# Performance work log

Hardware: AMD Instinct MI355X
Metric: run time of the kernel (lower is better)

The kernel has to match this reference:

```python
import jax, jax.numpy as jnp
import numpy as np
from jax import lax

_A = -0.75  # PyTorch bicubic coefficient


def _cubic_kernel(x):
    x = np.abs(x)
    return np.where(x <= 1.0, (_A + 2) * x**3 - (_A + 3) * x**2 + 1,
                    np.where(x < 2.0, _A * x**3 - 5 * _A * x**2 + 8 * _A * x - 4 * _A, 0.0))


def _cubic_mat(out_s, in_s):
    # align_corners=True bicubic interpolation matrix [out_s, in_s]
    i = np.arange(out_s)
    s = i * (in_s - 1) / (out_s - 1) if out_s > 1 else np.zeros(out_s)
    f = np.floor(s).astype(np.int64)
    t = s - f
    M = np.zeros((out_s, in_s), dtype=np.float32)
    for off in range(-1, 3):
        idx = np.clip(f + off, 0, in_s - 1)
        np.add.at(M, (i, idx), _cubic_kernel(t - off).astype(np.float32))
    return jnp.asarray(M)


def _bicubic_up(x, out_hw):
    Mh = _cubic_mat(out_hw[0], x.shape[-2])
    Mw = _cubic_mat(out_hw[1], x.shape[-1])
    y = jnp.einsum('Hh,bchw->bcHw', Mh, x)
    return jnp.einsum('Ww,bcHw->bcHW', Mw, y)


def _conv(x, w, b, pad=1):
    y = lax.conv_general_dilated(x, w, (1, 1), [(pad, pad), (pad, pad)],
                                 dimension_numbers=('NCHW', 'OIHW', 'NCHW'))
    return y + b[None, :, None, None]


def _pool(x):
    return lax.reduce_window(x, -jnp.inf, lax.max, (1, 1, 2, 2), (1, 1, 2, 2), 'VALID')


def _features(x, ws):
    # VGG19 feat1 = conv0+relu (64ch, full res); feat2 = conv2..conv14 (256ch, 1/4 res)
    x1 = jax.nn.relu(_conv(x, *ws[0]))
    h = jax.nn.relu(_conv(x1, *ws[1]))
    h = _pool(h)
    h = jax.nn.relu(_conv(h, *ws[2]))
    h = jax.nn.relu(_conv(h, *ws[3]))
    h = _pool(h)
    h = jax.nn.relu(_conv(h, *ws[4]))
    h = jax.nn.relu(_conv(h, *ws[5]))
    h = jax.nn.relu(_conv(h, *ws[6]))
    h = _bicubic_up(h, x1.shape[-2:])  # bicubic, align_corners=True
    return jnp.concatenate([x1, h], axis=1)  # 64 + 256 = 320 channels


def _forward(x_ref, x_template, w0, b0, w2, b2, w5, b5, w7, b7, w10, b10, w12, b12,
             w14, b14, coef_ref, coef_temp, fw1, fb1, fw2, fb2, fw3, fb3):
    ws = [(w0, b0), (w2, b2), (w5, b5), (w7, b7), (w10, b10), (w12, b12), (w14, b14)]
    fref = _features(x_ref, ws)
    ftem = _features(x_template, ws)
    # L2-normalize over channel dim
    fref = fref / (1e-8 + jnp.linalg.norm(fref, axis=1, keepdims=True))
    ftem = ftem / (1e-8 + jnp.linalg.norm(ftem, axis=1, keepdims=True))
    b, c, H, W = fref.shape
    fref = fref.reshape(b, c, H // 2, 2, W // 2, 2).mean(axis=(3, 5))
    # dense correlation volume
    dist = jnp.einsum('bcmn,bcpq->bmnpq', fref, ftem) / 320.0
    m, n, p, q = dist.shape[1:]
    dist = dist.reshape(b, m * n, p * q)
    # dual-axis softmax + sqrt combination (LoFTR-style)
    conf_ref = jax.nn.softmax(coef_ref * dist, axis=-2)
    conf_tmp = jax.nn.softmax(coef_temp * dist, axis=-1)
    confidence = jnp.sqrt(conf_ref * conf_tmp)
    conf_values, _ = lax.top_k(confidence, 5)  # [b, m*n, 5]
    conf = conf_values.reshape(b, m, n, 5).transpose(0, 3, 1, 2)
    # final head (dropout = identity in eval)
    h = jax.nn.relu(_conv(conf, fw1, fb1))
    h = jax.nn.relu(_conv(h, fw2, fb2))
    out = _conv(h, fw3, fb3, pad=0)
    out = _bicubic_up(out, x_ref.shape[-2:])
    return out


def setup_inputs() -> dict:
    key = jax.random.key(0)
    ks = jax.random.split(key, 16)
    B, H, W = 1, 128, 128

    def cw(k, o, i, s):
        return jax.random.normal(k, (o, i, s, s), jnp.float32) * (1.0 / np.sqrt(i * s * s))

    d = {
        'x_ref': jax.random.normal(ks[0], (B, 3, H, W), jnp.float32),
        'x_template': jax.random.normal(ks[1], (B, 3, H, W), jnp.float32),
        'w0': cw(ks[2], 64, 3, 3), 'b0': jnp.zeros((64,), jnp.float32),
        'w2': cw(ks[3], 64, 64, 3), 'b2': jnp.zeros((64,), jnp.float32),
        'w5': cw(ks[4], 128, 64, 3), 'b5': jnp.zeros((128,), jnp.float32),
        'w7': cw(ks[5], 128, 128, 3), 'b7': jnp.zeros((128,), jnp.float32),
        'w10': cw(ks[6], 256, 128, 3), 'b10': jnp.zeros((256,), jnp.float32),
        'w12': cw(ks[7], 256, 256, 3), 'b12': jnp.zeros((256,), jnp.float32),
        'w14': cw(ks[8], 256, 256, 3), 'b14': jnp.zeros((256,), jnp.float32),
        'coef_ref': jnp.float32(1.0), 'coef_temp': jnp.float32(1.0),
        # final head: weights_init_normal -> N(1/3, 0.02)
        'fw1': 1.0 / 3 + 0.02 * jax.random.normal(ks[9], (8, 5, 3, 3), jnp.float32),
        'fb1': 0.02 * jax.random.normal(ks[10], (8,), jnp.float32),
        'fw2': 1.0 / 3 + 0.02 * jax.random.normal(ks[11], (8, 8, 3, 3), jnp.float32),
        'fb2': 0.02 * jax.random.normal(ks[12], (8,), jnp.float32),
        'fw3': 1.0 / 3 + 0.02 * jax.random.normal(ks[13], (1, 8, 1, 1), jnp.float32),
        'fb3': 0.02 * jax.random.normal(ks[14], (1,), jnp.float32),
    }
    return d


def reference(x_ref, x_template, w0, b0, w2, b2, w5, b5, w7, b7, w10, b10, w12, b12,
              w14, b14, coef_ref, coef_temp, fw1, fb1, fw2, fb2, fw3, fb3):
    return _forward(x_ref, x_template, w0, b0, w2, b2, w5, b5, w7, b7, w10, b10,
                    w12, b12, w14, b14, coef_ref, coef_temp, fw1, fb1, fw2, fb2, fw3, fb3)
```

## Files before the change

### kernel.cpp

```cpp
#include <hip/hip_runtime.h>
#include <math.h>

typedef unsigned short ushort_t;
typedef unsigned int uint_t;
typedef __attribute__((ext_vector_type(8))) short bf16x8;
typedef __attribute__((ext_vector_type(4))) float f32x4;

#define FSTRIDE ((size_t)16384 * 320)
#define TSTRIDE ((size_t)16384 * 64)

__device__ inline ushort_t f2bf(float f) {
    union { float f; uint_t u; } x; x.f = f;
    uint_t r = x.u + 0x7fffu + ((x.u >> 16) & 1u);
    return (ushort_t)(r >> 16);
}
__device__ inline float bf2f(ushort_t h) {
    union { uint_t u; float f; } x; x.u = ((uint_t)h) << 16;
    return x.f;
}
__device__ inline float bflo(uint_t u) {
    union { uint_t u; float f; } x; x.u = u << 16; return x.f;
}
__device__ inline float bfhi(uint_t u) {
    union { uint_t u; float f; } x; x.u = u & 0xffff0000u; return x.f;
}

struct WT6 {
    const float* src[6];
    ushort_t* dst[6];
    int co[6], ci[6];
    int off[6];
};
__global__ void wtrans6_k(WT6 a)
{
    int b = blockIdx.x, seg = 0;
#pragma unroll
    for (int s = 1; s < 6; ++s) if (b >= a.off[s]) seg = s;
    int idx = (b - a.off[seg]) * 256 + threadIdx.x;
    int CO = a.co[seg], CI = a.ci[seg];
    if (idx >= CO * CI * 9) return;
    int tap = idx % 9;
    int rem = idx / 9;
    int ci = rem % CI;
    int co = rem / CI;
    a.dst[seg][((size_t)tap * CO + co) * CI + ci] = f2bf(a.src[seg][idx]);
}

__global__ __launch_bounds__(256) void conv0_k(const float* __restrict__ x0, const float* __restrict__ x1,
                                               const float* __restrict__ w,
                                               const float* __restrict__ b, ushort_t* __restrict__ F,
                                               ushort_t* __restrict__ t0)
{
    const float* x = blockIdx.y ? x1 : x0;
    F += (size_t)blockIdx.y * FSTRIDE;
    t0 += (size_t)blockIdx.y * TSTRIDE;
    int co = threadIdx.x & 63;
    int p = blockIdx.x * 4 + (threadIdx.x >> 6);
    int y = p >> 7, xx = p & 127;
    float acc = b[co];
#pragma unroll
    for (int ci = 0; ci < 3; ++ci) {
#pragma unroll
        for (int t = 0; t < 9; ++t) {
            int dy = t / 3 - 1, dx = t % 3 - 1;
            int yy = y + dy, xc = xx + dx;
            if ((unsigned)yy < 128u && (unsigned)xc < 128u) {
                acc += x[ci * 16384 + yy * 128 + xc] * w[co * 27 + ci * 9 + t];
            }
        }
    }
    ushort_t r = f2bf(fmaxf(acc, 0.f));
    F[(size_t)p * 320 + co] = r;
    t0[(size_t)p * 64 + co] = r;
}

template<int CI>
__global__ __launch_bounds__(256) void conv_mfma_k(
    const ushort_t* __restrict__ in, int ldin, int inoff, size_t inImgStride,
    const ushort_t* __restrict__ wT, const float* __restrict__ bias,
    ushort_t* __restrict__ out, int ldout, int outoff, size_t outImgStride,
    int H, int W, int CO)
{
    in += (size_t)blockIdx.z * inImgStride;
    out += (size_t)blockIdx.z * outImgStride;
    const int tid = threadIdx.x;
    const int lane = tid & 63, wid = tid >> 6;
    const int wr = wid >> 1, wc = wid & 1;
    const int m0 = blockIdx.x * 64;
    const int n0 = blockIdx.y * 64;
    const int fr = lane & 15;
    const int fo = (lane >> 4) << 3;

    size_t abase[2];
    unsigned vmask[2];
#pragma unroll
    for (int mi = 0; mi < 2; ++mi) {
        int p = m0 + wr * 32 + mi * 16 + fr;
        int y = p / W, x = p % W;
        abase[mi] = (size_t)p * ldin + inoff + fo;
        unsigned vm = 0;
#pragma unroll
        for (int t = 0; t < 9; ++t) {
            int dy = t / 3 - 1, dx = t % 3 - 1;
            if ((unsigned)(y + dy) < (unsigned)H && (unsigned)(x + dx) < (unsigned)W) vm |= 1u << t;
        }
        vmask[mi] = vm;
    }

    f32x4 zero = {0.f, 0.f, 0.f, 0.f};
    f32x4 acc[2][2] = {{zero, zero}, {zero, zero}};
    const bf16x8 zz = {0, 0, 0, 0, 0, 0, 0, 0};

    for (int t = 0; t < 9; ++t) {
        int toff = ((t / 3 - 1) * W + (t % 3 - 1)) * ldin;
        bool v0 = (vmask[0] >> t) & 1u;
        bool v1 = (vmask[1] >> t) & 1u;
        const ushort_t* wp0 = wT + ((size_t)(t * CO + n0 + wc * 32 + fr)) * CI + fo;
        const ushort_t* wp1 = wp0 + (size_t)16 * CI;
#pragma unroll
        for (int kc = 0; kc < CI / 32; ++kc) {
            int k0 = kc * 32;
            bf16x8 a0 = v0 ? *(const bf16x8*)(in + abase[0] + toff + k0) : zz;
            bf16x8 a1 = v1 ? *(const bf16x8*)(in + abase[1] + toff + k0) : zz;
            bf16x8 b0 = *(const bf16x8*)(wp0 + k0);
            bf16x8 b1 = *(const bf16x8*)(wp1 + k0);
            acc[0][0] = __builtin_amdgcn_mfma_f32_16x16x32_bf16(b0, a0, acc[0][0], 0, 0, 0);
            acc[0][1] = __builtin_amdgcn_mfma_f32_16x16x32_bf16(b1, a0, acc[0][1], 0, 0, 0);
            acc[1][0] = __builtin_amdgcn_mfma_f32_16x16x32_bf16(b0, a1, acc[1][0], 0, 0, 0);
            acc[1][1] = __builtin_amdgcn_mfma_f32_16x16x32_bf16(b1, a1, acc[1][1], 0, 0, 0);
        }
    }

#pragma unroll
    for (int mi = 0; mi < 2; ++mi) {
#pragma unroll
        for (int ni = 0; ni < 2; ++ni) {
            int pix = m0 + wr * 32 + mi * 16 + (lane & 15);
            int ch = n0 + wc * 32 + ni * 16 + ((lane >> 4) << 2);
            float4 bv = *(const float4*)(bias + ch);
            float r0 = fmaxf(acc[mi][ni][0] + bv.x, 0.f);
            float r1 = fmaxf(acc[mi][ni][1] + bv.y, 0.f);
            float r2 = fmaxf(acc[mi][ni][2] + bv.z, 0.f);
            float r3 = fmaxf(acc[mi][ni][3] + bv.w, 0.f);
            uint2 pk;
            pk.x = (uint_t)f2bf(r0) | ((uint_t)f2bf(r1) << 16);
            pk.y = (uint_t)f2bf(r2) | ((uint_t)f2bf(r3) << 16);
            *(uint2*)(out + (size_t)pix * ldout + outoff + ch) = pk;
        }
    }
}

template<int CI>
__global__ __launch_bounds__(128) void conv_mfma2w_k(
    const ushort_t* __restrict__ in, int ldin, size_t inImgStride,
    const ushort_t* __restrict__ wT, const float* __restrict__ bias,
    ushort_t* __restrict__ out, int ldout, size_t outImgStride,
    int H, int W, int CO)
{
    __shared__ float red[64][17];
    in += (size_t)blockIdx.z * inImgStride;
    out += (size_t)blockIdx.z * outImgStride;
    const int lane = threadIdx.x & 63;
    const int wv = threadIdx.x >> 6;
    const int m0 = blockIdx.x * 32;
    const int n0 = blockIdx.y * 32;
    const int fr = lane & 15;
    const int fo = (lane >> 4) << 3;

    size_t abase[2];
    unsigned vmask[2];
#pragma unroll
    for (int mi = 0; mi < 2; ++mi) {
        int p = m0 + mi * 16 + fr;
        int y = p / W, x = p % W;
        abase[mi] = (size_t)p * ldin + fo;
        unsigned vm = 0;
#pragma unroll
        for (int t = 0; t < 9; ++t) {
            int dy = t / 3 - 1, dx = t % 3 - 1;
            if ((unsigned)(y + dy) < (unsigned)H && (unsigned)(x + dx) < (unsigned)W) vm |= 1u << t;
        }
        vmask[mi] = vm;
    }

    f32x4 zero = {0.f, 0.f, 0.f, 0.f};
    f32x4 acc[2][2] = {{zero, zero}, {zero, zero}};
    const bf16x8 zz = {0, 0, 0, 0, 0, 0, 0, 0};

    const int tb = wv ? 5 : 0;
    const int te = wv ? 9 : 5;
    for (int t = tb; t < te; ++t) {
        int toff = ((t / 3 - 1) * W + (t % 3 - 1)) * ldin;
        bool v0 = (vmask[0] >> t) & 1u;
        bool v1 = (vmask[1] >> t) & 1u;
        const ushort_t* wp0 = wT + ((size_t)(t * CO + n0 + fr)) * CI + fo;
        const ushort_t* wp1 = wp0 + (size_t)16 * CI;
#pragma unroll
        for (int kc = 0; kc < CI / 32; ++kc) {
            int k0 = kc * 32;
            bf16x8 a0 = v0 ? *(const bf16x8*)(in + abase[0] + toff + k0) : zz;
            bf16x8 a1 = v1 ? *(const bf16x8*)(in + abase[1] + toff + k0) : zz;
            bf16x8 b0 = *(const bf16x8*)(wp0 + k0);
            bf16x8 b1 = *(const bf16x8*)(wp1 + k0);
            acc[0][0] = __builtin_amdgcn_mfma_f32_16x16x32_bf16(b0, a0, acc[0][0], 0, 0, 0);
            acc[0][1] = __builtin_amdgcn_mfma_f32_16x16x32_bf16(b1, a0, acc[0][1], 0, 0, 0);
            acc[1][0] = __builtin_amdgcn_mfma_f32_16x16x32_bf16(b0, a1, acc[1][0], 0, 0, 0);
            acc[1][1] = __builtin_amdgcn_mfma_f32_16x16x32_bf16(b1, a1, acc[1][1], 0, 0, 0);
        }
    }

    if (wv == 1) {
#pragma unroll
        for (int mi = 0; mi < 2; ++mi)
#pragma unroll
            for (int ni = 0; ni < 2; ++ni)
#pragma unroll
                for (int r = 0; r < 4; ++r)
                    red[lane][mi * 8 + ni * 4 + r] = acc[mi][ni][r];
    }
    __syncthreads();
    if (wv == 0) {
#pragma unroll
        for (int mi = 0; mi < 2; ++mi) {
#pragma unroll
            for (int ni = 0; ni < 2; ++ni) {
                int pix = m0 + mi * 16 + (lane & 15);
                int ch = n0 + ni * 16 + ((lane >> 4) << 2);
                float4 bv = *(const float4*)(bias + ch);
                float r0 = fmaxf(acc[mi][ni][0] + red[lane][mi * 8 + ni * 4 + 0] + bv.x, 0.f);
                float r1 = fmaxf(acc[mi][ni][1] + red[lane][mi * 8 + ni * 4 + 1] + bv.y, 0.f);
                float r2 = fmaxf(acc[mi][ni][2] + red[lane][mi * 8 + ni * 4 + 2] + bv.z, 0.f);
                float r3 = fmaxf(acc[mi][ni][3] + red[lane][mi * 8 + ni * 4 + 3] + bv.w, 0.f);
                uint2 pk;
                pk.x = (uint_t)f2bf(r0) | ((uint_t)f2bf(r1) << 16);
                pk.y = (uint_t)f2bf(r2) | ((uint_t)f2bf(r3) << 16);
                *(uint2*)(out + (size_t)pix * ldout + ch) = pk;
            }
        }
    }
}

__global__ void maxpool_nhwc_k(const ushort_t* __restrict__ in, ushort_t* __restrict__ out,
                               int C, int Hi, int Wi)
{
    in += (size_t)blockIdx.y * TSTRIDE;
    out += (size_t)blockIdx.y * TSTRIDE;
    int idx = blockIdx.x * 256 + threadIdx.x;
    int CG = C >> 3;
    int Wo = Wi >> 1, Ho = Hi >> 1;
    if (idx >= Ho * Wo * CG) return;
    int cg = idx % CG;
    int p = idx / CG;
    int y = p / Wo, x = p % Wo;
    const ushort_t* ip = in + ((size_t)(2 * y) * Wi + 2 * x) * C + cg * 8;
    bf16x8 v0 = *(const bf16x8*)(ip);
    bf16x8 v1 = *(const bf16x8*)(ip + C);
    bf16x8 v2 = *(const bf16x8*)(ip + (size_t)Wi * C);
    bf16x8 v3 = *(const bf16x8*)(ip + (size_t)Wi * C + C);
    bf16x8 r;
#pragma unroll
    for (int j = 0; j < 8; ++j) {
        float m = fmaxf(fmaxf(bf2f((ushort_t)v0[j]), bf2f((ushort_t)v1[j])),
                        fmaxf(bf2f((ushort_t)v2[j]), bf2f((ushort_t)v3[j])));
        r[j] = (short)f2bf(m);
    }
    *(bf16x8*)(out + (size_t)p * C + cg * 8) = r;
}

__device__ inline void cubw(float t, float* w) {
    float x0 = 1.f + t, x2 = 1.f - t, x3 = 2.f - t;
    w[0] = ((-0.75f*x0 + 3.75f)*x0 - 6.f)*x0 + 3.f;
    w[1] = (1.25f*t - 2.25f)*t*t + 1.f;
    w[2] = (1.25f*x2 - 2.25f)*x2*x2 + 1.f;
    w[3] = ((-0.75f*x3 + 3.75f)*x3 - 6.f)*x3 + 3.f;
}

__global__ __launch_bounds__(256) void upnorm_k(const ushort_t* __restrict__ in, ushort_t* __restrict__ F,
                                                ushort_t* __restrict__ Abuf)
{
    __shared__ float sm[4][320];
    in += (size_t)blockIdx.y * TSTRIDE;
    F += (size_t)blockIdx.y * FSTRIDE;
    int wid = threadIdx.x >> 6, lane = threadIdx.x & 63;
    int pb = blockIdx.x;
    int py = pb >> 6, px = pb & 63;
    int p = (2 * py + (wid >> 1)) * 128 + 2 * px + (wid & 1);
    int Y = p >> 7, X = p & 127;
    float sy = (float)Y * (31.f / 127.f);
    float sx = (float)X * (31.f / 127.f);
    int fy = (int)floorf(sy), fx = (int)floorf(sx);
    float ty = sy - (float)fy, tx = sx - (float)fx;
    float wy[4], wx[4];
    cubw(ty, wy); cubw(tx, wx);
    float a0 = 0.f, a1 = 0.f, a2 = 0.f, a3 = 0.f;
#pragma unroll
    for (int i = 0; i < 4; ++i) {
        int yy = min(max(fy - 1 + i, 0), 31);
#pragma unroll
        for (int j = 0; j < 4; ++j) {
            int xx = min(max(fx - 1 + j, 0), 31);
            float w = wy[i] * wx[j];
            uint2 v = *(const uint2*)(in + ((size_t)yy * 32 + xx) * 256 + lane * 4);
            a0 += w * bflo(v.x); a1 += w * bfhi(v.x);
            a2 += w * bflo(v.y); a3 += w * bfhi(v.y);
        }
    }
    float v0 = bf2f(f2bf(a0)), v1 = bf2f(f2bf(a1)), v2 = bf2f(f2bf(a2)), v3 = bf2f(f2bf(a3));
    float c0 = bf2f(F[(size_t)p * 320 + lane]);
    float ss = c0 * c0 + v0 * v0 + v1 * v1 + v2 * v2 + v3 * v3;
#pragma unroll
    for (int off = 32; off > 0; off >>= 1) ss += __shfl_xor(ss, off);
    float inv = 1.f / (1e-8f + sqrtf(ss));
    if (blockIdx.y == 1) {
        F[(size_t)p * 320 + lane] = f2bf(c0 * inv);
        uint2 pk;
        pk.x = (uint_t)f2bf(v0 * inv) | ((uint_t)f2bf(v1 * inv) << 16);
        pk.y = (uint_t)f2bf(v2 * inv) | ((uint_t)f2bf(v3 * inv) << 16);
        *(uint2*)(F + (size_t)p * 320 + 64 + lane * 4) = pk;
    } else {
        sm[wid][lane] = bf2f(f2bf(c0 * inv));
        sm[wid][64 + lane * 4 + 0] = bf2f(f2bf(v0 * inv));
        sm[wid][64 + lane * 4 + 1] = bf2f(f2bf(v1 * inv));
        sm[wid][64 + lane * 4 + 2] = bf2f(f2bf(v2 * inv));
        sm[wid][64 + lane * 4 + 3] = bf2f(f2bf(v3 * inv));
        __syncthreads();
        for (int ch = threadIdx.x; ch < 320; ch += 256) {
            float a = 0.25f * (sm[0][ch] + sm[1][ch] + sm[2][ch] + sm[3][ch]);
            Abuf[(size_t)pb * 320 + ch] = f2bf(a);
        }
    }
}

__global__ __launch_bounds__(256) void gemm_corr_k(
    const ushort_t* __restrict__ A, const ushort_t* __restrict__ B, char* __restrict__ D8,
    const float* __restrict__ coefr, const float* __restrict__ coeft,
    float* __restrict__ rpsum, float* __restrict__ cpsum)
{
    __shared__ ushort_t lA0[128 * 32];
    __shared__ ushort_t lB0[128 * 32];
    __shared__ ushort_t lA1[128 * 32];
    __shared__ ushort_t lB1[128 * 32];
    __shared__ float cl[2][128];
    __shared__ float rl[2][128];
    const int tid = threadIdx.x;
    const int lane = tid & 63;
    const int wid = tid >> 6;
    const int wr = wid >> 1, wc = wid & 1;
    const int m0 = blockIdx.y * 128, n0 = blockIdx.x * 128;
    const int fr = lane & 15;
    const int fo = (lane >> 4) << 3;
    const int srow = tid >> 2;
    const int scol = (tid & 3) << 3;

    const ushort_t* Ag0 = A + (size_t)(m0 + srow) * 320 + scol;
    const ushort_t* Ag1 = Ag0 + (size_t)64 * 320;
    const ushort_t* Bg0 = B + (size_t)(n0 + srow) * 320 + scol;
    const ushort_t* Bg1 = Bg0 + (size_t)64 * 320;

    f32x4 zero = {0.f, 0.f, 0.f, 0.f};
    f32x4 acc[4][4];
#pragma unroll
    for (int i = 0; i < 4; ++i)
#pragma unroll
        for (int j = 0; j < 4; ++j) acc[i][j] = zero;

    uint4 pA0, pA1, pB0, pB1;
    uint4 qA0, qA1, qB0, qB1;

#define GLOAD(rA0, rA1, rB0, rB1, kk) { \
        rA0 = *(const uint4*)(Ag0 + (kk)); \
        rA1 = *(const uint4*)(Ag1 + (kk)); \
        rB0 = *(const uint4*)(Bg0 + (kk)); \
        rB1 = *(const uint4*)(Bg1 + (kk)); }

#define DSW(LA, LB, rA0, rA1, rB0, rB1) { \
        *(uint4*)&LA[srow * 32 + scol] = rA0; \
        *(uint4*)&LA[(64 + srow) * 32 + scol] = rA1; \
        *(uint4*)&LB[srow * 32 + scol] = rB0; \
        *(uint4*)&LB[(64 + srow) * 32 + scol] = rB1; }

#define CMP(LA, LB) { \
        bf16x8 af[4], bfr[4]; \
        _Pragma("unroll") \
        for (int mi = 0; mi < 4; ++mi) \
            af[mi] = *(const bf16x8*)&LA[(wr * 64 + mi * 16 + fr) * 32 + fo]; \
        _Pragma("unroll") \
        for (int ni = 0; ni < 4; ++ni) \
            bfr[ni] = *(const bf16x8*)&LB[(wc * 64 + ni * 16 + fr) * 32 + fo]; \
        _Pragma("unroll") \
        for (int mi = 0; mi < 4; ++mi) \
            _Pragma("unroll") \
            for (int ni = 0; ni < 4; ++ni) \
                acc[mi][ni] = __builtin_amdgcn_mfma_f32_16x16x32_bf16(bfr[ni], af[mi], acc[mi][ni], 0, 0, 0); }

    GLOAD(pA0, pA1, pB0, pB1, 0)
    DSW(lA0, lB0, pA0, pA1, pB0, pB1)
    __syncthreads();

#pragma unroll
    for (int tt = 0; tt < 5; ++tt) {
        GLOAD(qA0, qA1, qB0, qB1, 32 * (2 * tt + 1))
        CMP(lA0, lB0)
        DSW(lA1, lB1, qA0, qA1, qB0, qB1)
        __syncthreads();
        if (tt < 4) {
            GLOAD(pA0, pA1, pB0, pB1, 32 * (2 * tt + 2))
            CMP(lA1, lB1)
            DSW(lA0, lB0, pA0, pA1, pB0, pB1)
            __syncthreads();
        } else {
            CMP(lA1, lB1)
        }
    }
#undef GLOAD
#undef DSW
#undef CMP

    const float s = 1.0f / 320.0f;
    const float cr = coefr[0], ct = coeft[0];
    const bool sameCoef = (cr == ct);
    float rpx[4] = {0.f, 0.f, 0.f, 0.f};
    float cpx[4][4];
#pragma unroll
    for (int ni = 0; ni < 4; ++ni)
#pragma unroll
        for (int r = 0; r < 4; ++r) cpx[ni][r] = 0.f;

    const int mrow = lane & 15;
    const int ng = (lane >> 4) << 2;
#pragma unroll
    for (int mi = 0; mi < 4; ++mi) {
        int m = m0 + wr * 64 + mi * 16 + mrow;
        char* drow = D8 + (size_t)m * 16384;
#pragma unroll
        for (int ni = 0; ni < 4; ++ni) {
            int n = n0 + wc * 64 + ni * 16 + ng;
            float d0 = acc[mi][ni][0] * s;
            float d1 = acc[mi][ni][1] * s;
            float d2 = acc[mi][ni][2] * s;
            float d3 = acc[mi][ni][3] * s;
            int q0 = __float2int_rn(fminf(fmaxf(d0 * 40640.f, -127.f), 127.f));
            int q1 = __float2int_rn(fminf(fmaxf(d1 * 40640.f, -127.f), 127.f));
            int q2 = __float2int_rn(fminf(fmaxf(d2 * 40640.f, -127.f), 127.f));
            int q3 = __float2int_rn(fminf(fmaxf(d3 * 40640.f, -127.f), 127.f));
            uint_t pk8 = (uint_t)(q0 & 255) | ((uint_t)(q1 & 255) << 8)
                       | ((uint_t)(q2 & 255) << 16) | ((uint_t)(q3 & 255) << 24);
            *(uint_t*)(drow + n) = pk8;
            float e0 = __expf(cr * d0), e1 = __expf(cr * d1);
            float e2 = __expf(cr * d2), e3 = __expf(cr * d3);
            cpx[ni][0] += e0; cpx[ni][1] += e1; cpx[ni][2] += e2; cpx[ni][3] += e3;
            if (sameCoef) {
                rpx[mi] += e0 + e1 + e2 + e3;
            } else {
                rpx[mi] += __expf(ct * d0) + __expf(ct * d1) + __expf(ct * d2) + __expf(ct * d3);
            }
        }
    }
#pragma unroll
    for (int mi = 0; mi < 4; ++mi) {
        rpx[mi] += __shfl_xor(rpx[mi], 16);
        rpx[mi] += __shfl_xor(rpx[mi], 32);
    }
    if (lane < 16) {
#pragma unroll
        for (int mi = 0; mi < 4; ++mi)
            rl[wc][wr * 64 + mi * 16 + lane] = rpx[mi];
    }
#pragma unroll
    for (int ni = 0; ni < 4; ++ni)
#pragma unroll
        for (int r = 0; r < 4; ++r) {
            cpx[ni][r] += __shfl_xor(cpx[ni][r], 1);
            cpx[ni][r] += __shfl_xor(cpx[ni][r], 2);
            cpx[ni][r] += __shfl_xor(cpx[ni][r], 4);
            cpx[ni][r] += __shfl_xor(cpx[ni][r], 8);
        }
    if ((lane & 15) == 0) {
        int g = lane >> 4;
#pragma unroll
        for (int ni = 0; ni < 4; ++ni)
#pragma unroll
            for (int r = 0; r < 4; ++r)
                cl[wr][wc * 64 + ni * 16 + g * 4 + r] = cpx[ni][r];
    }
    __syncthreads();
    if (tid < 128) {
        cpsum[(size_t)blockIdx.y * 16384 + n0 + tid] = cl[0][tid] + cl[1][tid];
        rpsum[(size_t)blockIdx.x * 4096 + m0 + tid] = rl[0][tid] + rl[1][tid];
    }
}

__global__ void finboth_k(const float* __restrict__ cpsum, const float* __restrict__ rpsum,
                          float* __restrict__ lc, float* __restrict__ invr)
{
    int b = blockIdx.x;
    if (b < 64) {
        int j = b * 256 + threadIdx.x;
        float s = 0.f;
#pragma unroll
        for (int k = 0; k < 32; ++k) s += cpsum[(size_t)k * 16384 + j];
        lc[j] = -0.5f * __logf(s);
    } else {
        int m = (b - 64) * 256 + threadIdx.x;
        float s = 0.f;
#pragma unroll
        for (int k = 0; k < 128; ++k) s += rpsum[(size_t)k * 4096 + m];
        invr[m] = rsqrtf(s);
    }
}

#define INS5(w_) { float w = (w_); float mx; \
    mx = fmaxf(w, t0); w = fminf(w, t0); t0 = mx; \
    mx = fmaxf(w, t1); w = fminf(w, t1); t1 = mx; \
    mx = fmaxf(w, t2); w = fminf(w, t2); t2 = mx; \
    mx = fmaxf(w, t3); w = fminf(w, t3); t3 = mx; \
    t4 = fmaxf(w, t4); }
#define SB(w, sft) ((float)(int)(signed char)(((w) >> (sft)) & 0xffu))

__global__ __launch_bounds__(256) void row_topk_k(
    const char* __restrict__ D8, const float* __restrict__ lc,
    const float* __restrict__ invr,
    const float* __restrict__ coefr, const float* __restrict__ coeft,
    float* __restrict__ conf5)
{
    int wid = threadIdx.x >> 6, lane = threadIdx.x & 63;
    int row = blockIdx.x * 4 + wid;
    float hc = 0.5f * (coefr[0] + coeft[0]);
    float hq = hc * (1.0f / 40640.f);
    const char* rp = D8 + (size_t)row * 16384;

    float t0 = -1e30f, t1 = -1e30f, t2 = -1e30f, t3 = -1e30f, t4 = -1e30f;
    for (int i = 0; i < 16; ++i) {
        int cw = i * 64 + lane;
        uint4 u = *(const uint4*)(rp + cw * 16);
        int col = cw * 16;
        float4 l0 = *(const float4*)(lc + col);
        float4 l1 = *(const float4*)(lc + col + 4);
        float4 l2 = *(const float4*)(lc + col + 8);
        float4 l3 = *(const float4*)(lc + col + 12);
        float k0  = fmaf(hq, SB(u.x, 0),  l0.x);
        float k1  = fmaf(hq, SB(u.x, 8),  l0.y);
        float k2  = fmaf(hq, SB(u.x, 16), l0.z);
        float k3  = fmaf(hq, SB(u.x, 24), l0.w);
        float k4  = fmaf(hq, SB(u.y, 0),  l1.x);
        float k5  = fmaf(hq, SB(u.y, 8),  l1.y);
        float k6  = fmaf(hq, SB(u.y, 16), l1.z);
        float k7  = fmaf(hq, SB(u.y, 24), l1.w);
        float k8  = fmaf(hq, SB(u.z, 0),  l2.x);
        float k9  = fmaf(hq, SB(u.z, 8),  l2.y);
        float k10 = fmaf(hq, SB(u.z, 16), l2.z);
        float k11 = fmaf(hq, SB(u.z, 24), l2.w);
        float k12 = fmaf(hq, SB(u.w, 0),  l3.x);
        float k13 = fmaf(hq, SB(u.w, 8),  l3.y);
        float k14 = fmaf(hq, SB(u.w, 16), l3.z);
        float k15 = fmaf(hq, SB(u.w, 24), l3.w);
        float ma = fmaxf(fmaxf(fmaxf(k0, k1), fmaxf(k2, k3)),
                         fmaxf(fmaxf(k4, k5), fmaxf(k6, k7)));
        float mb = fmaxf(fmaxf(fmaxf(k8, k9), fmaxf(k10, k11)),
                         fmaxf(fmaxf(k12, k13), fmaxf(k14, k15)));
        if (fmaxf(ma, mb) > t4) {
            INS5(k0);  INS5(k1);  INS5(k2);  INS5(k3);
            INS5(k4);  INS5(k5);  INS5(k6);  INS5(k7);
            INS5(k8);  INS5(k9);  INS5(k10); INS5(k11);
            INS5(k12); INS5(k13); INS5(k14); INS5(k15);
        }
    }
#pragma unroll
    for (int off = 1; off < 64; off <<= 1) {
        float o0 = __shfl_xor(t0, off), o1 = __shfl_xor(t1, off), o2 = __shfl_xor(t2, off);
        float o3 = __shfl_xor(t3, off), o4 = __shfl_xor(t4, off);
        INS5(o0); INS5(o1); INS5(o2); INS5(o3); INS5(o4);
    }
    if (lane == 0) {
        float iv = invr[row];
        conf5[0 * 4096 + row] = __expf(t0) * iv;
        conf5[1 * 4096 + row] = __expf(t1) * iv;
        conf5[2 * 4096 + row] = __expf(t2) * iv;
        conf5[3 * 4096 + row] = __expf(t3) * iv;
        conf5[4 * 4096 + row] = __expf(t4) * iv;
    }
}

__global__ void conv3x3_k(const float* __restrict__ in, const float* __restrict__ wgt,
                          const float* __restrict__ bias, float* __restrict__ out,
                          int Cin, int H, int W, int relu)
{
    int p = blockIdx.x * 256 + threadIdx.x;
    int HW = H * W;
    if (p >= HW) return;
    int co0 = blockIdx.y * 8;
    int y = p / W, x = p - y * W;
    float acc0 = bias[co0+0], acc1 = bias[co0+1], acc2 = bias[co0+2], acc3 = bias[co0+3];
    float acc4 = bias[co0+4], acc5 = bias[co0+5], acc6 = bias[co0+6], acc7 = bias[co0+7];
    bool ym = y > 0, yp = y < H-1, xm = x > 0, xp = x < W-1;
    for (int ci = 0; ci < Cin; ++ci) {
        const float* ip = in + (size_t)ci * HW + p;
        float v0 = (ym && xm) ? ip[-W-1] : 0.f;
        float v1 = (ym)       ? ip[-W]   : 0.f;
        float v2 = (ym && xp) ? ip[-W+1] : 0.f;
        float v3 = (xm)       ? ip[-1]   : 0.f;
        float v4 =              ip[0];
        float v5 = (xp)       ? ip[1]    : 0.f;
        float v6 = (yp && xm) ? ip[W-1]  : 0.f;
        float v7 = (yp)       ? ip[W]    : 0.f;
        float v8 = (yp && xp) ? ip[W+1]  : 0.f;
        const float* wp = wgt + ((size_t)co0 * Cin + ci) * 9;
        size_t ws = (size_t)Cin * 9;
#define CACC(q, a) { const float* wq = wp + q * ws; \
        a += wq[0]*v0 + wq[1]*v1 + wq[2]*v2 + wq[3]*v3 + wq[4]*v4 \
           + wq[5]*v5 + wq[6]*v6 + wq[7]*v7 + wq[8]*v8; }
        CACC(0, acc0) CACC(1, acc1) CACC(2, acc2) CACC(3, acc3)
        CACC(4, acc4) CACC(5, acc5) CACC(6, acc6) CACC(7, acc7)
#undef CACC
    }
#define CW(q, a) { float r = a; if (relu) r = fmaxf(r, 0.f); out[(size_t)(co0+q)*HW + p] = r; }
    CW(0, acc0) CW(1, acc1) CW(2, acc2) CW(3, acc3)
    CW(4, acc4) CW(5, acc5) CW(6, acc6) CW(7, acc7)
#undef CW
}

__global__ void head2_k(const float* __restrict__ in, const float* __restrict__ wgt,
                        const float* __restrict__ bias, const float* __restrict__ w3,
                        const float* __restrict__ b3, float* __restrict__ out64)
{
    int p = blockIdx.x * 256 + threadIdx.x;
    int y = p >> 6, x = p & 63;
    float acc[8];
#pragma unroll
    for (int c = 0; c < 8; ++c) acc[c] = bias[c];
    bool ym = y > 0, yp = y < 63, xm = x > 0, xp = x < 63;
#pragma unroll
    for (int ci = 0; ci < 8; ++ci) {
        const float* ip = in + ci * 4096 + p;
        float v0 = (ym && xm) ? ip[-65] : 0.f;
        float v1 = (ym)       ? ip[-64] : 0.f;
        float v2 = (ym && xp) ? ip[-63] : 0.f;
        float v3 = (xm)       ? ip[-1]  : 0.f;
        float v4 =              ip[0];
        float v5 = (xp)       ? ip[1]   : 0.f;
        float v6 = (yp && xm) ? ip[63]  : 0.f;
        float v7 = (yp)       ? ip[64]  : 0.f;
        float v8 = (yp && xp) ? ip[65]  : 0.f;
#pragma unroll
        for (int co = 0; co < 8; ++co) {
            const float* wq = wgt + ((size_t)co * 8 + ci) * 9;
            acc[co] += wq[0]*v0 + wq[1]*v1 + wq[2]*v2 + wq[3]*v3 + wq[4]*v4
                     + wq[5]*v5 + wq[6]*v6 + wq[7]*v7 + wq[8]*v8;
        }
    }
    float o = b3[0];
#pragma unroll
    for (int c = 0; c < 8; ++c) o += w3[c] * fmaxf(acc[c], 0.f);
    out64[p] = o;
}

__global__ void bicubic_k(const float* __restrict__ in, float* __restrict__ out,
                          int C, int Hin, int Win, int Hout, int Wout)
{
    int idx = blockIdx.x * 256 + threadIdx.x;
    int total = C * Hout * Wout;
    if (idx >= total) return;
    int X = idx % Wout;
    int Y = (idx / Wout) % Hout;
    int c = idx / (Wout * Hout);
    float sy = (float)Y * (float)(Hin - 1) / (float)(Hout - 1);
    float sx = (float)X * (float)(Win - 1) / (float)(Wout - 1);
    int fy = (int)floorf(sy), fx = (int)floorf(sx);
    float ty = sy - (float)fy, tx = sx - (float)fx;
    float wy[4], wx[4];
    cubw(ty, wy); cubw(tx, wx);
    const float* ip = in + (size_t)c * Hin * Win;
    float acc = 0.f;
#pragma unroll
    for (int i = 0; i < 4; ++i) {
        int yy = min(max(fy - 1 + i, 0), Hin - 1);
        float ra = 0.f;
#pragma unroll
        for (int j = 0; j < 4; ++j) {
            int xx = min(max(fx - 1 + j, 0), Hin == Win ? Win - 1 : Win - 1);
            ra += wx[j] * ip[yy * Win + xx];
        }
        acc += wy[i] * ra;
    }
    out[idx] = acc;
}

extern "C" void kernel_launch(void* const* d_in, const int* in_sizes, int n_in,
                              void* d_out, int out_size, void* d_ws, size_t ws_size,
                              hipStream_t stream)
{
    const float* x_ref = (const float*)d_in[0];
    const float* x_tem = (const float*)d_in[1];
    const float* w0  = (const float*)d_in[2];   const float* b0  = (const float*)d_in[3];
    const float* w2  = (const float*)d_in[4];   const float* b2  = (const float*)d_in[5];
    const float* w5  = (const float*)d_in[6];   const float* b5  = (const float*)d_in[7];
    const float* w7  = (const float*)d_in[8];   const float* b7  = (const float*)d_in[9];
    const float* w10 = (const float*)d_in[10];  const float* b10 = (const float*)d_in[11];
    const float* w12 = (const float*)d_in[12];  const float* b12 = (const float*)d_in[13];
    const float* w14 = (const float*)d_in[14];  const float* b14 = (const float*)d_in[15];
    const float* coefr = (const float*)d_in[16];
    const float* coeft = (const float*)d_in[17];
    const float* fw1 = (const float*)d_in[18];  const float* fb1 = (const float*)d_in[19];
    const float* fw2 = (const float*)d_in[20];  const float* fb2 = (const float*)d_in[21];
    const float* fw3 = (const float*)d_in[22];  const float* fb3 = (const float*)d_in[23];
    float* out = (float*)d_out;

    char* wsp = (char*)d_ws;
    auto alloc = [&](size_t bytes) { char* p = wsp; wsp += (bytes + 255) & ~(size_t)255; return p; };
    ushort_t* F     = (ushort_t*)alloc(2 * FSTRIDE * 2);
    ushort_t* t0    = (ushort_t*)alloc(2 * TSTRIDE * 2);
    ushort_t* t1    = (ushort_t*)alloc(2 * TSTRIDE * 2);
    ushort_t* t2    = (ushort_t*)alloc(2 * TSTRIDE * 2);
    ushort_t* wT2   = (ushort_t*)alloc((size_t)64 * 64 * 9 * 2);
    ushort_t* wT5   = (ushort_t*)alloc((size_t)128 * 64 * 9 * 2);
    ushort_t* wT7   = (ushort_t*)alloc((size_t)128 * 128 * 9 * 2);
    ushort_t* wT10  = (ushort_t*)alloc((size_t)256 * 128 * 9 * 2);
    ushort_t* wT12  = (ushort_t*)alloc((size_t)256 * 256 * 9 * 2);
    ushort_t* wT14  = (ushort_t*)alloc((size_t)256 * 256 * 9 * 2);
    ushort_t* Abuf  = (ushort_t*)alloc((size_t)4096 * 320 * 2);
    char*     dist8 = (char*)alloc((size_t)4096 * 16384);
    float*    rpsum = (float*)alloc((size_t)128 * 4096 * 4);
    float*    cpsum = (float*)alloc((size_t)32 * 16384 * 4);
    float*    lc    = (float*)alloc(16384 * 4);
    float*    invr  = (float*)alloc(4096 * 4);
    float*    conf5 = (float*)alloc(5 * 4096 * 4);
    float*    h1    = (float*)alloc(8 * 4096 * 4);
    float*    out64 = (float*)alloc(4096 * 4);
    (void)ws_size; (void)n_in; (void)in_sizes; (void)out_size;

    WT6 wt;
    wt.src[0] = w2;  wt.dst[0] = wT2;  wt.co[0] = 64;  wt.ci[0] = 64;
    wt.src[1] = w5;  wt.dst[1] = wT5;  wt.co[1] = 128; wt.ci[1] = 64;
    wt.src[2] = w7;  wt.dst[2] = wT7;  wt.co[2] = 128; wt.ci[2] = 128;
    wt.src[3] = w10; wt.dst[3] = wT10; wt.co[3] = 256; wt.ci[3] = 128;
    wt.src[4] = w12; wt.dst[4] = wT12; wt.co[4] = 256; wt.ci[4] = 256;
    wt.src[5] = w14; wt.dst[5] = wT14; wt.co[5] = 256; wt.ci[5] = 256;
    int nblk = 0;
    for (int s = 0; s < 6; ++s) { wt.off[s] = nblk; nblk += (wt.co[s] * wt.ci[s] * 9 + 255) / 256; }
    wtrans6_k<<<nblk, 256, 0, stream>>>(wt);

    conv0_k<<<dim3(4096, 2), 256, 0, stream>>>(x_ref, x_tem, w0, b0, F, t0);
    conv_mfma_k<64><<<dim3(256, 1, 2), 256, 0, stream>>>(t0, 64, 0, TSTRIDE, wT2, b2, t1, 64, 0, TSTRIDE, 128, 128, 64);
    maxpool_nhwc_k<<<dim3(128, 2), 256, 0, stream>>>(t1, t2, 64, 128, 128);
    conv_mfma_k<64><<<dim3(64, 2, 2), 256, 0, stream>>>(t2, 64, 0, TSTRIDE, wT5, b5, t1, 128, 0, TSTRIDE, 64, 64, 128);
    conv_mfma_k<128><<<dim3(64, 2, 2), 256, 0, stream>>>(t1, 128, 0, TSTRIDE, wT7, b7, t2, 128, 0, TSTRIDE, 64, 64, 128);
    maxpool_nhwc_k<<<dim3(64, 2), 256, 0, stream>>>(t2, t1, 128, 64, 64);
    conv_mfma2w_k<128><<<dim3(32, 8, 2), 128, 0, stream>>>(t1, 128, TSTRIDE, wT10, b10, t2, 256, TSTRIDE, 32, 32, 256);
    conv_mfma2w_k<256><<<dim3(32, 8, 2), 128, 0, stream>>>(t2, 256, TSTRIDE, wT12, b12, t1, 256, TSTRIDE, 32, 32, 256);
    conv_mfma2w_k<256><<<dim3(32, 8, 2), 128, 0, stream>>>(t1, 256, TSTRIDE, wT14, b14, t2, 256, TSTRIDE, 32, 32, 256);
    upnorm_k<<<dim3(4096, 2), 256, 0, stream>>>(t2, F, Abuf);

    gemm_corr_k<<<dim3(128, 32), 256, 0, stream>>>(Abuf, F + FSTRIDE, dist8, coefr, coeft, rpsum, cpsum);

    finboth_k<<<80, 256, 0, stream>>>(cpsum, rpsum, lc, invr);

    row_topk_k<<<1024, 256, 0, stream>>>(dist8, lc, invr, coefr, coeft, conf5);

    conv3x3_k<<<dim3(16, 1), 256, 0, stream>>>(conf5, fw1, fb1, h1, 5, 64, 64, 1);
    head2_k<<<16, 256, 0, stream>>>(h1, fw2, fb2, fw3, fb3, out64);
    bicubic_k<<<64, 256, 0, stream>>>(out64, out, 1, 64, 64, 128, 128);
}
```

Before: 386.6 us.

## Restructure correlation GEMM to keep A panel resident in LDS and stream B

The correlation GEMM now runs 512 blocks. Each block loads a full 64x320 A panel into padded LDS once, then loops over 2048 columns of B, loading B fragments directly from global memory into registers without LDS staging or barriers. The grid is swizzled so that neighbouring blocks share B columns. Partial-sum layouts change to match: 64 column partials and 8 row partials, and the finalize kernel is updated accordingly. This removes the per-K-step LDS double buffering and syncs, but B is read from global with less reuse, and the serial 16-iteration loop per block lowers parallelism.

```diff
diff --git a/kernel.cpp b/kernel.cpp
--- a/kernel.cpp
+++ b/kernel.cpp
@@ -336,157 +336,124 @@
     const float* __restrict__ coefr, const float* __restrict__ coeft,
     float* __restrict__ rpsum, float* __restrict__ cpsum)
 {
-    __shared__ ushort_t lA0[128 * 32];
-    __shared__ ushort_t lB0[128 * 32];
-    __shared__ ushort_t lA1[128 * 32];
-    __shared__ ushort_t lB1[128 * 32];
-    __shared__ float cl[2][128];
-    __shared__ float rl[2][128];
+    __shared__ ushort_t lA[64 * 328];
+    __shared__ float rl[4][64];
     const int tid = threadIdx.x;
     const int lane = tid & 63;
-    const int wid = tid >> 6;
-    const int wr = wid >> 1, wc = wid & 1;
-    const int m0 = blockIdx.y * 128, n0 = blockIdx.x * 128;
+    const int wv = tid >> 6;
     const int fr = lane & 15;
     const int fo = (lane >> 4) << 3;
-    const int srow = tid >> 2;
-    const int scol = (tid & 3) << 3;
-
-    const ushort_t* Ag0 = A + (size_t)(m0 + srow) * 320 + scol;
-    const ushort_t* Ag1 = Ag0 + (size_t)64 * 320;
-    const ushort_t* Bg0 = B + (size_t)(n0 + srow) * 320 + scol;
-    const ushort_t* Bg1 = Bg0 + (size_t)64 * 320;
-
-    f32x4 zero = {0.f, 0.f, 0.f, 0.f};
-    f32x4 acc[4][4];
-#pragma unroll
-    for (int i = 0; i < 4; ++i)
-#pragma unroll
-        for (int j = 0; j < 4; ++j) acc[i][j] = zero;
-
-    uint4 pA0, pA1, pB0, pB1;
-    uint4 qA0, qA1, qB0, qB1;
-
-#define GLOAD(rA0, rA1, rB0, rB1, kk) { \
-        rA0 = *(const uint4*)(Ag0 + (kk)); \
-        rA1 = *(const uint4*)(Ag1 + (kk)); \
-        rB0 = *(const uint4*)(Bg0 + (kk)); \
-        rB1 = *(const uint4*)(Bg1 + (kk)); }
-
-#define DSW(LA, LB, rA0, rA1, rB0, rB1) { \
-        *(uint4*)&LA[srow * 32 + scol] = rA0; \
-        *(uint4*)&LA[(64 + srow) * 32 + scol] = rA1; \
-        *(uint4*)&LB[srow * 32 + scol] = rB0; \
-        *(uint4*)&LB[(64 + srow) * 32 + scol] = rB1; }
-
-#define CMP(LA, LB) { \
-        bf16x8 af[4], bfr[4]; \
-        _Pragma("unroll") \
-        for (int mi = 0; mi < 4; ++mi) \
-            af[mi] = *(const bf16x8*)&LA[(wr * 64 + mi * 16 + fr) * 32 + fo]; \
-        _Pragma("unroll") \
-        for (int ni = 0; ni < 4; ++ni) \
-            bfr[ni] = *(const bf16x8*)&LB[(wc * 64 + ni * 16 + fr) * 32 + fo]; \
-        _Pragma("unroll") \
-        for (int mi = 0; mi < 4; ++mi) \
-            _Pragma("unroll") \
-            for (int ni = 0; ni < 4; ++ni) \
-                acc[mi][ni] = __builtin_amdgcn_mfma_f32_16x16x32_bf16(bfr[ni], af[mi], acc[mi][ni], 0, 0, 0); }
-
-    GLOAD(pA0, pA1, pB0, pB1, 0)
-    DSW(lA0, lB0, pA0, pA1, pB0, pB1)
+    const int ng = (lane >> 4) << 2;
+
+    int bid = blockIdx.x;
+    int swz = (bid & 7) * 64 + (bid >> 3);
+    const int mb = swz & 63;
+    const int nc = swz >> 6;
+
+#pragma unroll
+    for (int i = 0; i < 10; ++i) {
+        int e = (i * 256 + tid) * 8;
+        int row = e / 320, col = e % 320;
+        uint4 v = *(const uint4*)(A + ((size_t)(mb * 64 + row)) * 320 + col);
+        *(uint4*)&lA[row * 328 + col] = v;
+    }
     __syncthreads();
-
-#pragma unroll
-    for (int tt = 0; tt < 5; ++tt) {
-        GLOAD(qA0, qA1, qB0, qB1, 32 * (2 * tt + 1))
-        CMP(lA0, lB0)
-        DSW(lA1, lB1, qA0, qA1, qB0, qB1)
-        __syncthreads();
-        if (tt < 4) {
-            GLOAD(pA0, pA1, pB0, pB1, 32 * (2 * tt + 2))
-            CMP(lA1, lB1)
-            DSW(lA0, lB0, pA0, pA1, pB0, pB1)
-            __syncthreads();
-        } else {
-            CMP(lA1, lB1)
-        }
-    }
-#undef GLOAD
-#undef DSW
-#undef CMP
 
     const float s = 1.0f / 320.0f;
     const float cr = coefr[0], ct = coeft[0];
     const bool sameCoef = (cr == ct);
-    float rpx[4] = {0.f, 0.f, 0.f, 0.f};
-    float cpx[4][4];
-#pragma unroll
-    for (int ni = 0; ni < 4; ++ni)
-#pragma unroll
-        for (int r = 0; r < 4; ++r) cpx[ni][r] = 0.f;
-
-    const int mrow = lane & 15;
-    const int ng = (lane >> 4) << 2;
-#pragma unroll
-    for (int mi = 0; mi < 4; ++mi) {
-        int m = m0 + wr * 64 + mi * 16 + mrow;
-        char* drow = D8 + (size_t)m * 16384;
-#pragma unroll
-        for (int ni = 0; ni < 4; ++ni) {
-            int n = n0 + wc * 64 + ni * 16 + ng;
-            float d0 = acc[mi][ni][0] * s;
-            float d1 = acc[mi][ni][1] * s;
-            float d2 = acc[mi][ni][2] * s;
-            float d3 = acc[mi][ni][3] * s;
-            int q0 = __float2int_rn(fminf(fmaxf(d0 * 40640.f, -127.f), 127.f));
-            int q1 = __float2int_rn(fminf(fmaxf(d1 * 40640.f, -127.f), 127.f));
-            int q2 = __float2int_rn(fminf(fmaxf(d2 * 40640.f, -127.f), 127.f));
-            int q3 = __float2int_rn(fminf(fmaxf(d3 * 40640.f, -127.f), 127.f));
-            uint_t pk8 = (uint_t)(q0 & 255) | ((uint_t)(q1 & 255) << 8)
-                       | ((uint_t)(q2 & 255) << 16) | ((uint_t)(q3 & 255) << 24);
-            *(uint_t*)(drow + n) = pk8;
-            float e0 = __expf(cr * d0), e1 = __expf(cr * d1);
-            float e2 = __expf(cr * d2), e3 = __expf(cr * d3);
-            cpx[ni][0] += e0; cpx[ni][1] += e1; cpx[ni][2] += e2; cpx[ni][3] += e3;
-            if (sameCoef) {
-                rpx[mi] += e0 + e1 + e2 + e3;
-            } else {
-                rpx[mi] += __expf(ct * d0) + __expf(ct * d1) + __expf(ct * d2) + __expf(ct * d3);
+    float rpx0 = 0.f, rpx1 = 0.f, rpx2 = 0.f, rpx3 = 0.f;
+
+    for (int it = 0; it < 16; ++it) {
+        const int n0 = nc * 2048 + it * 128 + wv * 32;
+        const ushort_t* Bg0 = B + (size_t)(n0 + fr) * 320 + fo;
+        const ushort_t* Bg1 = Bg0 + (size_t)16 * 320;
+
+        f32x4 zero = {0.f, 0.f, 0.f, 0.f};
+        f32x4 acc[4][2];
+#pragma unroll
+        for (int mi = 0; mi < 4; ++mi) { acc[mi][0] = zero; acc[mi][1] = zero; }
+
+#pragma unroll
+        for (int kk = 0; kk < 10; ++kk) {
+            const int k0 = kk * 32;
+            bf16x8 b0 = *(const bf16x8*)(Bg0 + k0);
+            bf16x8 b1 = *(const bf16x8*)(Bg1 + k0);
+#pragma unroll
+            for (int mi = 0; mi < 4; ++mi) {
+                bf16x8 af = *(const bf16x8*)&lA[(mi * 16 + fr) * 328 + k0 + fo];
+                acc[mi][0] = __builtin_amdgcn_mfma_f32_16x16x32_bf16(b0, af, acc[mi][0], 0, 0, 0);
+                acc[mi][1] = __builtin_amdgcn_mfma_f32_16x16x32_bf16(b1, af, acc[mi][1], 0, 0, 0);
             }
         }
-    }
-#pragma unroll
-    for (int mi = 0; mi < 4; ++mi) {
-        rpx[mi] += __shfl_xor(rpx[mi], 16);
-        rpx[mi] += __shfl_xor(rpx[mi], 32);
-    }
+
+        float cpx[2][4];
+#pragma unroll
+        for (int nf = 0; nf < 2; ++nf)
+#pragma unroll
+            for (int r = 0; r < 4; ++r) cpx[nf][r] = 0.f;
+
+#pragma unroll
+        for (int mi = 0; mi < 4; ++mi) {
+            int m = mb * 64 + mi * 16 + (lane & 15);
+            char* drow = D8 + (size_t)m * 16384;
+#pragma unroll
+            for (int nf = 0; nf < 2; ++nf) {
+                int n = n0 + nf * 16 + ng;
+                float d0 = acc[mi][nf][0] * s;
+                float d1 = acc[mi][nf][1] * s;
+                float d2 = acc[mi][nf][2] * s;
+                float d3 = acc[mi][nf][3] * s;
+                int q0 = __float2int_rn(fminf(fmaxf(d0 * 40640.f, -127.f), 127.f));
+                int q1 = __float2int_rn(fminf(fmaxf(d1 * 40640.f, -127.f), 127.f));
+                int q2 = __float2int_rn(fminf(fmaxf(d2 * 40640.f, -127.f), 127.f));
+                int q3 = __float2int_rn(fminf(fmaxf(d3 * 40640.f, -127.f), 127.f));
+                uint_t pk8 = (uint_t)(q0 & 255) | ((uint_t)(q1 & 255) << 8)
+                           | ((uint_t)(q2 & 255) << 16) | ((uint_t)(q3 & 255) << 24);
+                *(uint_t*)(drow + n) = pk8;
+                float e0 = __expf(cr * d0), e1 = __expf(cr * d1);
+                float e2 = __expf(cr * d2), e3 = __expf(cr * d3);
+                cpx[nf][0] += e0; cpx[nf][1] += e1; cpx[nf][2] += e2; cpx[nf][3] += e3;
+                float re;
+                if (sameCoef) re = e0 + e1 + e2 + e3;
+                else re = __expf(ct * d0) + __expf(ct * d1) + __expf(ct * d2) + __expf(ct * d3);
+                if (mi == 0) rpx0 += re; else if (mi == 1) rpx1 += re;
+                else if (mi == 2) rpx2 += re; else rpx3 += re;
+            }
+        }
+#pragma unroll
+        for (int nf = 0; nf < 2; ++nf)
+#pragma unroll
+            for (int r = 0; r < 4; ++r) {
+                cpx[nf][r] += __shfl_xor(cpx[nf][r], 1);
+                cpx[nf][r] += __shfl_xor(cpx[nf][r], 2);
+                cpx[nf][r] += __shfl_xor(cpx[nf][r], 4);
+                cpx[nf][r] += __shfl_xor(cpx[nf][r], 8);
+            }
+        if ((lane & 15) == 0) {
+            int g = lane >> 4;
+#pragma unroll
+            for (int nf = 0; nf < 2; ++nf)
+#pragma unroll
+                for (int r = 0; r < 4; ++r)
+                    cpsum[(size_t)mb * 16384 + n0 + nf * 16 + g * 4 + r] = cpx[nf][r];
+        }
+    }
+
+    rpx0 += __shfl_xor(rpx0, 16); rpx0 += __shfl_xor(rpx0, 32);
+    rpx1 += __shfl_xor(rpx1, 16); rpx1 += __shfl_xor(rpx1, 32);
+    rpx2 += __shfl_xor(rpx2, 16); rpx2 += __shfl_xor(rpx2, 32);
+    rpx3 += __shfl_xor(rpx3, 16); rpx3 += __shfl_xor(rpx3, 32);
     if (lane < 16) {
-#pragma unroll
-        for (int mi = 0; mi < 4; ++mi)
-            rl[wc][wr * 64 + mi * 16 + lane] = rpx[mi];
-    }
-#pragma unroll
-    for (int ni = 0; ni < 4; ++ni)
-#pragma unroll
-        for (int r = 0; r < 4; ++r) {
-            cpx[ni][r] += __shfl_xor(cpx[ni][r], 1);
-            cpx[ni][r] += __shfl_xor(cpx[ni][r], 2);
-            cpx[ni][r] += __shfl_xor(cpx[ni][r], 4);
-            cpx[ni][r] += __shfl_xor(cpx[ni][r], 8);
-        }
-    if ((lane & 15) == 0) {
-        int g = lane >> 4;
-#pragma unroll
-        for (int ni = 0; ni < 4; ++ni)
-#pragma unroll
-            for (int r = 0; r < 4; ++r)
-                cl[wr][wc * 64 + ni * 16 + g * 4 + r] = cpx[ni][r];
+        rl[wv][0 * 16 + lane] = rpx0;
+        rl[wv][1 * 16 + lane] = rpx1;
+        rl[wv][2 * 16 + lane] = rpx2;
+        rl[wv][3 * 16 + lane] = rpx3;
     }
     __syncthreads();
-    if (tid < 128) {
-        cpsum[(size_t)blockIdx.y * 16384 + n0 + tid] = cl[0][tid] + cl[1][tid];
-        rpsum[(size_t)blockIdx.x * 4096 + m0 + tid] = rl[0][tid] + rl[1][tid];
+    if (tid < 64) {
+        float rsum = rl[0][tid] + rl[1][tid] + rl[2][tid] + rl[3][tid];
+        rpsum[(size_t)nc * 4096 + mb * 64 + tid] = rsum;
     }
 }
 
@@ -498,13 +465,13 @@
         int j = b * 256 + threadIdx.x;
         float s = 0.f;
 #pragma unroll
-        for (int k = 0; k < 32; ++k) s += cpsum[(size_t)k * 16384 + j];
+        for (int k = 0; k < 64; ++k) s += cpsum[(size_t)k * 16384 + j];
         lc[j] = -0.5f * __logf(s);
     } else {
         int m = (b - 64) * 256 + threadIdx.x;
         float s = 0.f;
 #pragma unroll
-        for (int k = 0; k < 128; ++k) s += rpsum[(size_t)k * 4096 + m];
+        for (int k = 0; k < 8; ++k) s += rpsum[(size_t)k * 4096 + m];
         invr[m] = rsqrtf(s);
     }
 }
@@ -677,7 +644,7 @@
         float ra = 0.f;
 #pragma unroll
         for (int j = 0; j < 4; ++j) {
-            int xx = min(max(fx - 1 + j, 0), Hin == Win ? Win - 1 : Win - 1);
+            int xx = min(max(fx - 1 + j, 0), Win - 1);
             ra += wx[j] * ip[yy * Win + xx];
         }
         acc += wy[i] * ra;
@@ -719,8 +686,8 @@
     ushort_t* wT14  = (ushort_t*)alloc((size_t)256 * 256 * 9 * 2);
     ushort_t* Abuf  = (ushort_t*)alloc((size_t)4096 * 320 * 2);
     char*     dist8 = (char*)alloc((size_t)4096 * 16384);
-    float*    rpsum = (float*)alloc((size_t)128 * 4096 * 4);
-    float*    cpsum = (float*)alloc((size_t)32 * 16384 * 4);
+    float*    rpsum = (float*)alloc((size_t)8 * 4096 * 4);
+    float*    cpsum = (float*)alloc((size_t)64 * 16384 * 4);
     float*    lc    = (float*)alloc(16384 * 4);
     float*    invr  = (float*)alloc(4096 * 4);
     float*    conf5 = (float*)alloc(5 * 4096 * 4);
@@ -750,7 +717,7 @@
     conv_mfma2w_k<256><<<dim3(32, 8, 2), 128, 0, stream>>>(t1, 256, TSTRIDE, wT14, b14, t2, 256, TSTRIDE, 32, 32, 256);
     upnorm_k<<<dim3(4096, 2), 256, 0, stream>>>(t2, F, Abuf);
 
-    gemm_corr_k<<<dim3(128, 32), 256, 0, stream>>>(Abuf, F + FSTRIDE, dist8, coefr, coeft, rpsum, cpsum);
+    gemm_corr_k<<<512, 256, 0, stream>>>(Abuf, F + FSTRIDE, dist8, coefr, coeft, rpsum, cpsum);
 
     finboth_k<<<80, 256, 0, stream>>>(cpsum, rpsum, lc, invr);
 
```

New measurement: 400.5 us. +3.6%, slower.
